# Optimization experiments

Hardware: AMD Instinct MI355X
Metric: run time of the kernel (lower is better)

The kernel has to match this reference:

```python
import jax, jax.numpy as jnp
import numpy as np

S, B, D, H, V, MF = 50, 128, 512, 512, 30000, 32
PAD = 0


def setup_inputs() -> dict:
    key = jax.random.key(0)
    ks = jax.random.split(key, 10)
    inp = {
        "user": jax.random.normal(ks[0], (B, MF), dtype=jnp.float32),
        "item": jax.random.normal(ks[1], (B, MF), dtype=jnp.float32),
        "review_input": jax.random.randint(ks[2], (S, B), 0, V, dtype=jnp.int64),
        "review_target": jax.random.randint(ks[3], (S, B), 0, V, dtype=jnp.int64),
        # learned parameters
        "word_emb": jax.random.normal(ks[4], (V, D), dtype=jnp.float32) * 0.02,
        "W_ih": jax.random.normal(ks[5], (3 * H, D), dtype=jnp.float32) * (1.0 / np.sqrt(D)),
        "W_hh": jax.random.normal(ks[6], (3 * H, H), dtype=jnp.float32) * (1.0 / np.sqrt(H)),
        "b_ih": jnp.zeros((3 * H,), dtype=jnp.float32),
        "b_hh": jnp.zeros((3 * H,), dtype=jnp.float32),
        "W_out": jax.random.normal(ks[7], (V, H), dtype=jnp.float32) * (1.0 / np.sqrt(H)),
        "b_out": jnp.zeros((V,), dtype=jnp.float32),
    }
    return inp


def _gru_forward(review_input, word_emb, W_ih, W_hh, b_ih, b_hh, W_out, b_out, batch):
    Hdim = W_hh.shape[1]
    h0 = jnp.zeros((batch, Hdim), dtype=word_emb.dtype)  # encoder returns zeros
    x = word_emb[review_input]  # [S, B, D] embedding lookup (dropout is identity in eval)

    def step(h, x_t):
        gi = x_t @ W_ih.T + b_ih            # [B, 3H]
        gh = h @ W_hh.T + b_hh              # [B, 3H]
        i_r, i_z, i_n = jnp.split(gi, 3, axis=-1)
        h_r, h_z, h_n = jnp.split(gh, 3, axis=-1)
        r = jax.nn.sigmoid(i_r + h_r)
        z = jax.nn.sigmoid(i_z + h_z)
        n = jnp.tanh(i_n + r * h_n)
        h_new = (1.0 - z) * n + z * h
        return h_new, h_new

    _, hs = jax.lax.scan(step, h0, x)       # [S, B, H]
    logits = jnp.einsum('sbh,vh->sbv', hs, W_out) + b_out  # decode from hidden_state
    return logits.reshape(-1, W_out.shape[0])  # [S*B, V], same row order as torch.cat


def reference(user, item, review_input, review_target, word_emb, W_ih, W_hh,
              b_ih, b_hh, W_out, b_out):
    batch = user.shape[0]
    logits = _gru_forward(review_input, word_emb, W_ih, W_hh, b_ih, b_hh,
                          W_out, b_out, batch)
    targets = review_target.reshape(-1)                     # [S*B]
    logp = jax.nn.log_softmax(logits, axis=-1)
    nll = -jnp.take_along_axis(logp, targets[:, None], axis=-1)[:, 0]
    mask = (targets != PAD)
    out_loss = jnp.where(mask, nll, 0.0)                    # reduction='none', ignore_index=PAD
    denom = jnp.maximum(jnp.sum(mask.astype(logits.dtype)), 1.0)
    obj = jnp.sum(out_loss) / denom                         # mean over non-pad tokens
    return (out_loss, obj)
```

## Files before the change

kernel.cpp:

```cpp
#include <hip/hip_runtime.h>
#include <hip/hip_bf16.h>

typedef __attribute__((ext_vector_type(8))) short short8;
typedef __attribute__((ext_vector_type(4))) float floatx4;

#define S_LEN  50
#define BATCH  128
#define DIM    512
#define HID    512
#define G3     1536
#define VOCAB  30000
#define TOKENS 6400
#define NB256  118
#define NVC    472
#define NWG    (25 * NB256)

#define N8_WIH   (G3 * DIM / 8)
#define N8_WHH   (G3 * HID / 8)
#define N8_WOUT  (VOCAB * DIM / 8)
#define N8_GATH  (TOKENS * DIM / 8)
#define N8_TOTAL (N8_WIH + N8_WHH + N8_WOUT + N8_GATH)

__device__ __forceinline__ float bf2f(short u) {
    union { unsigned int i; float f; } c;
    c.i = ((unsigned int)(unsigned short)u) << 16;
    return c.f;
}
__device__ __forceinline__ unsigned short f2bf(float x) {
    __hip_bfloat16 h = __float2bfloat16(x);
    unsigned short u;
    __builtin_memcpy(&u, &h, 2);
    return u;
}
__device__ __forceinline__ void gl_lds16(const void* g, void* l) {
    __builtin_amdgcn_global_load_lds(
        (const __attribute__((address_space(1))) void*)g,
        (__attribute__((address_space(3))) void*)l, 16, 0, 0);
}

__global__ void k_prep(const float* __restrict__ Wih, const float* __restrict__ Whh,
                       const float* __restrict__ Wout, const float* __restrict__ emb,
                       const int* __restrict__ idx,
                       unsigned short* __restrict__ WihB, unsigned short* __restrict__ WhhB,
                       unsigned short* __restrict__ WoutB, unsigned short* __restrict__ X) {
    int g = blockIdx.x * 256 + threadIdx.x;
    const float* src;
    unsigned short* dst;
    if (g < N8_WIH) {
        src = Wih + (size_t)g * 8;  dst = WihB + (size_t)g * 8;
    } else if (g < N8_WIH + N8_WHH) {
        int h = g - N8_WIH;
        src = Whh + (size_t)h * 8;  dst = WhhB + (size_t)h * 8;
    } else if (g < N8_WIH + N8_WHH + N8_WOUT) {
        int h = g - (N8_WIH + N8_WHH);
        src = Wout + (size_t)h * 8; dst = WoutB + (size_t)h * 8;
    } else {
        int h = g - (N8_WIH + N8_WHH + N8_WOUT);
        int token = h >> 6;
        int chunk = (h & 63) << 3;
        src = emb + (size_t)idx[token] * DIM + chunk;
        dst = X + (size_t)token * DIM + chunk;
    }
    union { short8 v; unsigned short u[8]; } o;
#pragma unroll
    for (int i = 0; i < 8; ++i) o.u[i] = f2bf(src[i]);
    *(short8*)dst = o.v;
}

__launch_bounds__(256)
__global__ void k_gemm_gi(const unsigned short* __restrict__ X,
                          const unsigned short* __restrict__ Wih,
                          const float* __restrict__ b_ih,
                          float* __restrict__ GI) {
    __shared__ unsigned short As[128 * 64];
    __shared__ unsigned short Bs[128 * 64];
    int bid = blockIdx.x;
    int wgid = (bid % 8) * 75 + bid / 8;
    int mb = wgid % 50, nb = wgid / 50;
    int m0 = mb * 128, n0 = nb * 128;

    int t = threadIdx.x, w = t >> 6, lane = t & 63;
    int wr = w >> 1, wc = w & 1;

    floatx4 zero = {0.f, 0.f, 0.f, 0.f};
    floatx4 acc[4][4];
#pragma unroll
    for (int mi = 0; mi < 4; ++mi)
#pragma unroll
        for (int ni = 0; ni < 4; ++ni) acc[mi][ni] = zero;

    int srow = t >> 1;
    int scq  = (t & 1) * 32;
    const unsigned short* gA = X   + (size_t)(m0 + srow) * DIM + scq;
    const unsigned short* gB = Wih + (size_t)(n0 + srow) * DIM + scq;
    int wo[4];
#pragma unroll
    for (int q = 0; q < 4; ++q)
        wo[q] = (srow * 128 + scq * 2 + q * 16) ^ ((srow & 7) << 4);

    for (int k0 = 0; k0 < DIM; k0 += 64) {
#pragma unroll
        for (int q = 0; q < 4; ++q) {
            *(short8*)((char*)As + wo[q]) = *(const short8*)(gA + k0 + q * 8);
            *(short8*)((char*)Bs + wo[q]) = *(const short8*)(gB + k0 + q * 8);
        }
        __syncthreads();
#pragma unroll
        for (int kt = 0; kt < 2; ++kt) {
            short8 af[4], bf[4];
#pragma unroll
            for (int mi = 0; mi < 4; ++mi) {
                int row = wr * 64 + mi * 16 + (lane & 15);
                int off = (row * 128 + kt * 64 + (lane >> 4) * 16) ^ ((row & 7) << 4);
                af[mi] = *(const short8*)((const char*)As + off);
            }
#pragma unroll
            for (int ni = 0; ni < 4; ++ni) {
                int row = wc * 64 + ni * 16 + (lane & 15);
                int off = (row * 128 + kt * 64 + (lane >> 4) * 16) ^ ((row & 7) << 4);
                bf[ni] = *(const short8*)((const char*)Bs + off);
            }
#pragma unroll
            for (int mi = 0; mi < 4; ++mi)
#pragma unroll
                for (int ni = 0; ni < 4; ++ni)
                    acc[mi][ni] = __builtin_amdgcn_mfma_f32_16x16x32_bf16(af[mi], bf[ni], acc[mi][ni], 0, 0, 0);
        }
        __syncthreads();
    }
#pragma unroll
    for (int mi = 0; mi < 4; ++mi)
#pragma unroll
        for (int ni = 0; ni < 4; ++ni) {
            int col = n0 + wc * 64 + ni * 16 + (lane & 15);
            float bo = b_ih[col];
#pragma unroll
            for (int r = 0; r < 4; ++r) {
                int row = m0 + wr * 64 + mi * 16 + (lane >> 4) * 4 + r;
                GI[(size_t)row * G3 + col] = acc[mi][ni][r] + bo;
            }
        }
}

__launch_bounds__(64)
__global__ void k_gru_step(const float* __restrict__ GI,
                           const unsigned short* __restrict__ Whh,
                           const float* __restrict__ b_hh,
                           float* __restrict__ hf,
                           const unsigned short* __restrict__ hin,
                           unsigned short* __restrict__ hout,
                           int s) {
    int lane = threadIdx.x & 63;
    int bg = blockIdx.x & 7;
    int hs = blockIdx.x >> 3;
    int jc = hs * 16 + (lane & 15);

    floatx4 acc0 = {0.f, 0.f, 0.f, 0.f};
    floatx4 acc1 = {0.f, 0.f, 0.f, 0.f};
    floatx4 acc2 = {0.f, 0.f, 0.f, 0.f};
    if (s != 0) {
        const unsigned short* pa  = hin + (size_t)(bg * 16 + (lane & 15)) * HID + (lane >> 4) * 8;
        const unsigned short* pb0 = Whh + (size_t)(0 * HID + jc) * DIM + (lane >> 4) * 8;
        const unsigned short* pb1 = Whh + (size_t)(1 * HID + jc) * DIM + (lane >> 4) * 8;
        const unsigned short* pb2 = Whh + (size_t)(2 * HID + jc) * DIM + (lane >> 4) * 8;
#pragma unroll
        for (int kt = 0; kt < 16; ++kt) {
            short8 a = *(const short8*)(pa + kt * 32);
            acc0 = __builtin_amdgcn_mfma_f32_16x16x32_bf16(a, *(const short8*)(pb0 + kt * 32), acc0, 0, 0, 0);
            acc1 = __builtin_amdgcn_mfma_f32_16x16x32_bf16(a, *(const short8*)(pb1 + kt * 32), acc1, 0, 0, 0);
            acc2 = __builtin_amdgcn_mfma_f32_16x16x32_bf16(a, *(const short8*)(pb2 + kt * 32), acc2, 0, 0, 0);
        }
    }
    float bhr = b_hh[jc], bhz = b_hh[jc + 512], bhn = b_hh[jc + 1024];
#pragma unroll
    for (int r = 0; r < 4; ++r) {
        int brow = bg * 16 + (lane >> 4) * 4 + r;
        int tok = s * BATCH + brow;
        const float* gi = GI + (size_t)tok * G3;
        float rg = 1.f / (1.f + __expf(-(gi[jc] + acc0[r] + bhr)));
        float zg = 1.f / (1.f + __expf(-(gi[jc + 512] + acc1[r] + bhz)));
        float ng = tanhf(gi[jc + 1024] + rg * (acc2[r] + bhn));
        size_t hidx = (size_t)brow * HID + jc;
        float hn = (1.f - zg) * ng + zg * hf[hidx];
        hf[hidx] = hn;
        hout[hidx] = f2bf(hn);
    }
}

__launch_bounds__(1024, 4)
__global__ void k_decode(const unsigned short* __restrict__ HS,
                         const unsigned short* __restrict__ Wout,
                         const float* __restrict__ b_out,
                         float* __restrict__ partial) {
    __shared__ unsigned short As[2][256 * 64];
    __shared__ unsigned short Bs[2][256 * 64];

    int bid = blockIdx.x;
    int xcd = bid & 7, pos = bid >> 3;
    int p = (xcd < 6 ? xcd * 369 : 2214 + (xcd - 6) * 368) + pos;
    int sgrp = p / 200;
    int rr   = p - sgrp * 200;
    int mb, nb;
    if (sgrp < 14) { mb = rr >> 3; nb = sgrp * 8 + (rr & 7); }
    else           { int q6 = rr / 6; mb = q6; nb = 112 + (rr - q6 * 6); }
    int m0 = mb * 256, n0 = nb * 256;

    int t = threadIdx.x, w = t >> 6, lane = t & 63;
    int wr = w >> 2, wc = w & 3;

    floatx4 zero = {0.f, 0.f, 0.f, 0.f};
    floatx4 acc[4][4];
#pragma unroll
    for (int mi = 0; mi < 4; ++mi)
#pragma unroll
        for (int ni = 0; ni < 4; ++ni) acc[mi][ni] = zero;

    int r8  = lane >> 3;
    int cbs = ((lane & 7) ^ r8) * 16;
    int c0 = w * 2, c1 = c0 + 1;
    int rA0 = c0 * 8 + r8, rA1 = c1 * 8 + r8;
    const char* gA0 = (const char*)(HS + (size_t)(m0 + rA0) * DIM) + cbs;
    const char* gA1 = (const char*)(HS + (size_t)(m0 + rA1) * DIM) + cbs;
    int v0 = n0 + rA0; if (v0 > VOCAB - 1) v0 = VOCAB - 1;
    int v1 = n0 + rA1; if (v1 > VOCAB - 1) v1 = VOCAB - 1;
    const char* gB0 = (const char*)(Wout + (size_t)v0 * DIM) + cbs;
    const char* gB1 = (const char*)(Wout + (size_t)v1 * DIM) + cbs;

    int roA[4][2], roB[4][2];
#pragma unroll
    for (int mi = 0; mi < 4; ++mi)
#pragma unroll
        for (int kh = 0; kh < 2; ++kh) {
            int row = wr * 64 + mi * 16 + (lane & 15);
            roA[mi][kh] = (row * 128 + kh * 64 + (lane >> 4) * 16) ^ ((row & 7) << 4);
        }
#pragma unroll
    for (int ni = 0; ni < 4; ++ni)
#pragma unroll
        for (int kh = 0; kh < 2; ++kh) {
            int row = wc * 64 + ni * 16 + (lane & 15);
            roB[ni][kh] = (row * 128 + kh * 64 + (lane >> 4) * 16) ^ ((row & 7) << 4);
        }

#define STAGE(kt, buf) do { int ko_ = (kt) * 128;                        \
        gl_lds16(gA0 + ko_, (char*)As[buf] + c0 * 1024);                 \
        gl_lds16(gA1 + ko_, (char*)As[buf] + c1 * 1024);                 \
        gl_lds16(gB0 + ko_, (char*)Bs[buf] + c0 * 1024);                 \
        gl_lds16(gB1 + ko_, (char*)Bs[buf] + c1 * 1024); } while (0)

    STAGE(0, 0);
    __builtin_amdgcn_sched_barrier(0);

    for (int kt = 0; kt < 8; ++kt) {
        int cur = kt & 1;
        if (kt < 7) {
            STAGE(kt + 1, cur ^ 1);
            __builtin_amdgcn_sched_barrier(0);
            asm volatile("s_waitcnt vmcnt(4)" ::: "memory");
        } else {
            asm volatile("s_waitcnt vmcnt(0)" ::: "memory");
        }
        __builtin_amdgcn_sched_barrier(0);
        __builtin_amdgcn_s_barrier();
        __builtin_amdgcn_sched_barrier(0);
#pragma unroll
        for (int kh = 0; kh < 2; ++kh) {
            short8 af[4], bf[4];
#pragma unroll
            for (int mi = 0; mi < 4; ++mi)
                af[mi] = *(const short8*)((const char*)As[cur] + roA[mi][kh]);
#pragma unroll
            for (int ni = 0; ni < 4; ++ni)
                bf[ni] = *(const short8*)((const char*)Bs[cur] + roB[ni][kh]);
#pragma unroll
            for (int mi = 0; mi < 4; ++mi)
#pragma unroll
                for (int ni = 0; ni < 4; ++ni)
                    acc[mi][ni] = __builtin_amdgcn_mfma_f32_16x16x32_bf16(af[mi], bf[ni], acc[mi][ni], 0, 0, 0);
        }
        __builtin_amdgcn_sched_barrier(0);
        __builtin_amdgcn_s_barrier();
        __builtin_amdgcn_sched_barrier(0);
    }
#undef STAGE

    float esum[4][4];
#pragma unroll
    for (int mi = 0; mi < 4; ++mi)
#pragma unroll
        for (int r = 0; r < 4; ++r) esum[mi][r] = 0.f;
#pragma unroll
    for (int ni = 0; ni < 4; ++ni) {
        int v = n0 + wc * 64 + ni * 16 + (lane & 15);
        bool ok = v < VOCAB;
        float bo = ok ? b_out[v] : 0.f;
#pragma unroll
        for (int mi = 0; mi < 4; ++mi)
#pragma unroll
            for (int r = 0; r < 4; ++r) {
                float logit = acc[mi][ni][r] + bo;
                esum[mi][r] += ok ? __expf(logit) : 0.f;
            }
    }
#pragma unroll
    for (int d = 1; d < 16; d <<= 1)
#pragma unroll
        for (int mi = 0; mi < 4; ++mi)
#pragma unroll
            for (int r = 0; r < 4; ++r) esum[mi][r] += __shfl_xor(esum[mi][r], d, 64);
    if ((lane & 15) == 0) {
#pragma unroll
        for (int mi = 0; mi < 4; ++mi)
#pragma unroll
            for (int r = 0; r < 4; ++r) {
                int tok = m0 + wr * 64 + mi * 16 + (lane >> 4) * 4 + r;
                partial[(size_t)tok * 512 + nb * 4 + wc] = esum[mi][r];
            }
    }
}

__global__ void k_lse_tlg(const float* __restrict__ partial,
                          const unsigned short* __restrict__ HS,
                          const unsigned short* __restrict__ Wout,
                          const float* __restrict__ b_out,
                          const int* __restrict__ target,
                          float* __restrict__ lse, float* __restrict__ tlg) {
    int tok = blockIdx.x * 4 + (threadIdx.x >> 6);
    int lane = threadIdx.x & 63;
    int tg = target[tok];
    short8 a = *(const short8*)(HS + (size_t)tok * DIM + lane * 8);
    short8 b = *(const short8*)(Wout + (size_t)tg * DIM + lane * 8);
    float s = 0.f;
#pragma unroll
    for (int i = 0; i < 8; ++i) s += bf2f(a[i]) * bf2f(b[i]);
    float s2 = 0.f;
    for (int j = lane; j < NVC; j += 64) s2 += partial[(size_t)tok * 512 + j];
#pragma unroll
    for (int d = 1; d < 64; d <<= 1) {
        s  += __shfl_xor(s, d, 64);
        s2 += __shfl_xor(s2, d, 64);
    }
    if (lane == 0) {
        tlg[tok] = s + b_out[tg];
        lse[tok] = logf(s2);
    }
}

__global__ void k_finalize(const float* __restrict__ lse, const float* __restrict__ tlg,
                           const int* __restrict__ target, float* __restrict__ out) {
    __shared__ float ssum[256];
    __shared__ float scnt[256];
    int t = threadIdx.x;
    float ls = 0.f, lc = 0.f;
    for (int i = t; i < TOKENS; i += 256) {
        int tg = target[i];
        float loss = (tg != 0) ? (lse[i] - tlg[i]) : 0.f;
        out[i] = loss;
        ls += loss;
        lc += (tg != 0) ? 1.f : 0.f;
    }
    ssum[t] = ls; scnt[t] = lc;
    __syncthreads();
    for (int d = 128; d > 0; d >>= 1) {
        if (t < d) { ssum[t] += ssum[t + d]; scnt[t] += scnt[t + d]; }
        __syncthreads();
    }
    if (t == 0) out[TOKENS] = ssum[0] / fmaxf(scnt[0], 1.f);
}

extern "C" void kernel_launch(void* const* d_in, const int* in_sizes, int n_in,
                              void* d_out, int out_size, void* d_ws, size_t ws_size,
                              hipStream_t stream) {
    const int*   review_input  = (const int*)d_in[2];
    const int*   review_target = (const int*)d_in[3];
    const float* word_emb      = (const float*)d_in[4];
    const float* W_ih          = (const float*)d_in[5];
    const float* W_hh          = (const float*)d_in[6];
    const float* b_ih          = (const float*)d_in[7];
    const float* b_hh          = (const float*)d_in[8];
    const float* W_out         = (const float*)d_in[9];
    const float* b_out         = (const float*)d_in[10];
    float* out = (float*)d_out;

    char* ws = (char*)d_ws;
    size_t off = 0;
    auto alloc = [&](size_t n) { char* p = ws + off; off += (n + 255) & ~(size_t)255; return p; };
    unsigned short* Xb    = (unsigned short*)alloc((size_t)TOKENS * DIM * 2);
    unsigned short* Wihb  = (unsigned short*)alloc((size_t)G3 * DIM * 2);
    unsigned short* Whhb  = (unsigned short*)alloc((size_t)G3 * HID * 2);
    unsigned short* Woutb = (unsigned short*)alloc((size_t)VOCAB * DIM * 2);
    unsigned short* HS    = (unsigned short*)alloc((size_t)TOKENS * HID * 2);
    float* hf      = (float*)alloc((size_t)BATCH * HID * 4);
    float* GI      = (float*)alloc((size_t)TOKENS * G3 * 4);
    float* partial = (float*)alloc((size_t)TOKENS * 512 * 4);
    float* lse     = (float*)alloc((size_t)TOKENS * 4);
    float* tlg     = (float*)alloc((size_t)TOKENS * 4);
    (void)ws_size; (void)in_sizes; (void)n_in; (void)out_size;

    k_prep<<<dim3(N8_TOTAL / 256), dim3(256), 0, stream>>>(
        W_ih, W_hh, W_out, word_emb, review_input, Wihb, Whhb, Woutb, Xb);

    k_gemm_gi<<<dim3(600), dim3(256), 0, stream>>>(Xb, Wihb, b_ih, GI);

    hipMemsetAsync(hf, 0, (size_t)BATCH * HID * 4, stream);
    for (int s = 0; s < S_LEN; ++s) {
        const unsigned short* hin = s ? (HS + (size_t)(s - 1) * BATCH * HID) : HS;
        unsigned short* hout = HS + (size_t)s * BATCH * HID;
        k_gru_step<<<dim3(256), dim3(64), 0, stream>>>(GI, Whhb, b_hh, hf, hin, hout, s);
    }

    k_decode<<<dim3(NWG), dim3(1024), 0, stream>>>(HS, Woutb, b_out, partial);
    k_lse_tlg<<<dim3(TOKENS / 4), dim3(256), 0, stream>>>(partial, HS, Woutb, b_out, review_target, lse, tlg);
    k_finalize<<<dim3(1), dim3(256), 0, stream>>>(lse, tlg, review_target, out);
}
```

Measured before the change: 553.6 us.

## Halve decode waves per block with larger per-wave tiles and MFMA priority

The decode GEMM block shrinks from 16 waves to 8. Each wave now computes 128x64 of the 256x256 output tile instead of 64x64, and issues four A and four B global-to-LDS loads per stage. This raises register reuse of B fragments and lowers the LDS-read-to-MFMA ratio. s_setprio is also raised around the MFMA section. In exchange, each wave holds twice the accumulators, which raises register pressure and may reduce occupancy or cause spills. There are also fewer waves to hide load latency.

```diff
diff --git a/kernel.cpp b/kernel.cpp
--- a/kernel.cpp
+++ b/kernel.cpp
@@ -187,7 +187,7 @@
     }
 }
 
-__launch_bounds__(1024, 4)
+__launch_bounds__(512)
 __global__ void k_decode(const unsigned short* __restrict__ HS,
                          const unsigned short* __restrict__ Wout,
                          const float* __restrict__ b_out,
@@ -209,29 +209,34 @@
     int wr = w >> 2, wc = w & 3;
 
     floatx4 zero = {0.f, 0.f, 0.f, 0.f};
-    floatx4 acc[4][4];
-#pragma unroll
-    for (int mi = 0; mi < 4; ++mi)
+    floatx4 acc[8][4];
+#pragma unroll
+    for (int mi = 0; mi < 8; ++mi)
 #pragma unroll
         for (int ni = 0; ni < 4; ++ni) acc[mi][ni] = zero;
 
     int r8  = lane >> 3;
     int cbs = ((lane & 7) ^ r8) * 16;
-    int c0 = w * 2, c1 = c0 + 1;
-    int rA0 = c0 * 8 + r8, rA1 = c1 * 8 + r8;
-    const char* gA0 = (const char*)(HS + (size_t)(m0 + rA0) * DIM) + cbs;
-    const char* gA1 = (const char*)(HS + (size_t)(m0 + rA1) * DIM) + cbs;
-    int v0 = n0 + rA0; if (v0 > VOCAB - 1) v0 = VOCAB - 1;
-    int v1 = n0 + rA1; if (v1 > VOCAB - 1) v1 = VOCAB - 1;
-    const char* gB0 = (const char*)(Wout + (size_t)v0 * DIM) + cbs;
-    const char* gB1 = (const char*)(Wout + (size_t)v1 * DIM) + cbs;
-
-    int roA[4][2], roB[4][2];
-#pragma unroll
-    for (int mi = 0; mi < 4; ++mi)
+    const char* gAq[4];
+    const char* gBq[4];
+#pragma unroll
+    for (int q = 0; q < 4; ++q) {
+        int chunk = w * 4 + q;
+        int row = chunk * 8 + r8;
+        gAq[q] = (const char*)(HS + (size_t)(m0 + row) * DIM) + cbs;
+        int v = n0 + row; if (v > VOCAB - 1) v = VOCAB - 1;
+        gBq[q] = (const char*)(Wout + (size_t)v * DIM) + cbs;
+    }
+    int ldsoff[4];
+#pragma unroll
+    for (int q = 0; q < 4; ++q) ldsoff[q] = (w * 4 + q) * 1024;
+
+    int roA[8][2], roB[4][2];
+#pragma unroll
+    for (int mi = 0; mi < 8; ++mi)
 #pragma unroll
         for (int kh = 0; kh < 2; ++kh) {
-            int row = wr * 64 + mi * 16 + (lane & 15);
+            int row = wr * 128 + mi * 16 + (lane & 15);
             roA[mi][kh] = (row * 128 + kh * 64 + (lane >> 4) * 16) ^ ((row & 7) << 4);
         }
 #pragma unroll
@@ -242,11 +247,15 @@
             roB[ni][kh] = (row * 128 + kh * 64 + (lane >> 4) * 16) ^ ((row & 7) << 4);
         }
 
-#define STAGE(kt, buf) do { int ko_ = (kt) * 128;                        \
-        gl_lds16(gA0 + ko_, (char*)As[buf] + c0 * 1024);                 \
-        gl_lds16(gA1 + ko_, (char*)As[buf] + c1 * 1024);                 \
-        gl_lds16(gB0 + ko_, (char*)Bs[buf] + c0 * 1024);                 \
-        gl_lds16(gB1 + ko_, (char*)Bs[buf] + c1 * 1024); } while (0)
+#define STAGE(kt, buf) do { int ko_ = (kt) * 128;                          \
+        gl_lds16(gAq[0] + ko_, (char*)As[buf] + ldsoff[0]);                \
+        gl_lds16(gAq[1] + ko_, (char*)As[buf] + ldsoff[1]);                \
+        gl_lds16(gAq[2] + ko_, (char*)As[buf] + ldsoff[2]);                \
+        gl_lds16(gAq[3] + ko_, (char*)As[buf] + ldsoff[3]);                \
+        gl_lds16(gBq[0] + ko_, (char*)Bs[buf] + ldsoff[0]);                \
+        gl_lds16(gBq[1] + ko_, (char*)Bs[buf] + ldsoff[1]);                \
+        gl_lds16(gBq[2] + ko_, (char*)Bs[buf] + ldsoff[2]);                \
+        gl_lds16(gBq[3] + ko_, (char*)Bs[buf] + ldsoff[3]); } while (0)
 
     STAGE(0, 0);
     __builtin_amdgcn_sched_barrier(0);
@@ -256,37 +265,39 @@
         if (kt < 7) {
             STAGE(kt + 1, cur ^ 1);
             __builtin_amdgcn_sched_barrier(0);
-            asm volatile("s_waitcnt vmcnt(4)" ::: "memory");
+            asm volatile("s_waitcnt vmcnt(8)" ::: "memory");
         } else {
             asm volatile("s_waitcnt vmcnt(0)" ::: "memory");
         }
         __builtin_amdgcn_sched_barrier(0);
         __builtin_amdgcn_s_barrier();
         __builtin_amdgcn_sched_barrier(0);
+        __builtin_amdgcn_s_setprio(1);
 #pragma unroll
         for (int kh = 0; kh < 2; ++kh) {
-            short8 af[4], bf[4];
-#pragma unroll
-            for (int mi = 0; mi < 4; ++mi)
+            short8 af[8], bf[4];
+#pragma unroll
+            for (int mi = 0; mi < 8; ++mi)
                 af[mi] = *(const short8*)((const char*)As[cur] + roA[mi][kh]);
 #pragma unroll
             for (int ni = 0; ni < 4; ++ni)
                 bf[ni] = *(const short8*)((const char*)Bs[cur] + roB[ni][kh]);
 #pragma unroll
-            for (int mi = 0; mi < 4; ++mi)
+            for (int mi = 0; mi < 8; ++mi)
 #pragma unroll
                 for (int ni = 0; ni < 4; ++ni)
                     acc[mi][ni] = __builtin_amdgcn_mfma_f32_16x16x32_bf16(af[mi], bf[ni], acc[mi][ni], 0, 0, 0);
         }
+        __builtin_amdgcn_s_setprio(0);
         __builtin_amdgcn_sched_barrier(0);
         __builtin_amdgcn_s_barrier();
         __builtin_amdgcn_sched_barrier(0);
     }
 #undef STAGE
 
-    float esum[4][4];
-#pragma unroll
-    for (int mi = 0; mi < 4; ++mi)
+    float esum[8][4];
+#pragma unroll
+    for (int mi = 0; mi < 8; ++mi)
 #pragma unroll
         for (int r = 0; r < 4; ++r) esum[mi][r] = 0.f;
 #pragma unroll
@@ -295,7 +306,7 @@
         bool ok = v < VOCAB;
         float bo = ok ? b_out[v] : 0.f;
 #pragma unroll
-        for (int mi = 0; mi < 4; ++mi)
+        for (int mi = 0; mi < 8; ++mi)
 #pragma unroll
             for (int r = 0; r < 4; ++r) {
                 float logit = acc[mi][ni][r] + bo;
@@ -305,15 +316,15 @@
 #pragma unroll
     for (int d = 1; d < 16; d <<= 1)
 #pragma unroll
-        for (int mi = 0; mi < 4; ++mi)
+        for (int mi = 0; mi < 8; ++mi)
 #pragma unroll
             for (int r = 0; r < 4; ++r) esum[mi][r] += __shfl_xor(esum[mi][r], d, 64);
     if ((lane & 15) == 0) {
 #pragma unroll
-        for (int mi = 0; mi < 4; ++mi)
+        for (int mi = 0; mi < 8; ++mi)
 #pragma unroll
             for (int r = 0; r < 4; ++r) {
-                int tok = m0 + wr * 64 + mi * 16 + (lane >> 4) * 4 + r;
+                int tok = m0 + wr * 128 + mi * 16 + (lane >> 4) * 4 + r;
                 partial[(size_t)tok * 512 + nb * 4 + wc] = esum[mi][r];
             }
     }
@@ -409,7 +420,7 @@
         k_gru_step<<<dim3(256), dim3(64), 0, stream>>>(GI, Whhb, b_hh, hf, hin, hout, s);
     }
 
-    k_decode<<<dim3(NWG), dim3(1024), 0, stream>>>(HS, Woutb, b_out, partial);
+    k_decode<<<dim3(NWG), dim3(512), 0, stream>>>(HS, Woutb, b_out, partial);
     k_lse_tlg<<<dim3(TOKENS / 4), dim3(256), 0, stream>>>(partial, HS, Woutb, b_out, review_target, lse, tlg);
     k_finalize<<<dim3(1), dim3(256), 0, stream>>>(lse, tlg, review_target, out);
 }
```

Result: slower. 579.4 us (+4.7%).
